# Performance work log

Measured on AMD Instinct MI355X. Metric: run time of the kernel, lower is better.

## Reference

```python
import jax, jax.numpy as jnp
import numpy as np

B, C, E = 2, 1024, 1024
H = 16            # n_heads as declared (used as per-group feature dim due to module's reshape)
HD = E // H       # 64 — the axis actually batched over in attention


def setup_inputs() -> dict:
    key = jax.random.key(0)
    ks = jax.random.split(key, 5)
    scale = 0.02
    return {
        "x": jax.random.normal(ks[0], (B, C, E), dtype=jnp.float32),
        "W_q": jax.random.normal(ks[1], (E, E), dtype=jnp.float32) * scale,
        "W_k": jax.random.normal(ks[2], (E, E), dtype=jnp.float32) * scale,
        "W_v": jax.random.normal(ks[3], (E, E), dtype=jnp.float32) * scale,
        "W_o": jax.random.normal(ks[4], (E, E), dtype=jnp.float32) * scale,
    }


def reference(x, W_q, W_k, W_v, W_o):
    # nn.Linear: y = x @ W.T  (bias=False)
    def proj_split(W):
        y = jnp.einsum('bce,de->bcd', x, W)              # [B,C,E]
        # view(B, C, HD, H).transpose(1,2) -> [B, HD, C, H]  (faithful to source layout)
        return y.reshape(B, C, HD, H).transpose(0, 2, 1, 3)

    Q = proj_split(W_q)
    K = proj_split(W_k)
    V = proj_split(W_v)

    scale = 1.0 / jnp.sqrt(jnp.asarray(H, dtype=x.dtype))  # sqrt of last dim (= n_heads here)
    scores = jnp.einsum('bdqh,bdkh->bdqk', Q, K) * scale    # [B, HD, C, C]
    weights = jax.nn.softmax(scores, axis=-1)
    out = jnp.einsum('bdqk,bdkh->bdqh', weights, V)         # [B, HD, C, H]
    out = out.transpose(0, 2, 1, 3).reshape(B, C, E)        # [B, C, E]
    out = jnp.einsum('bce,de->bcd', out, W_o)
    return out  # dropout p=0.0 / eval mode: identity
```

## Files before the change

kernel.cpp:

```cpp
#include <hip/hip_runtime.h>
#include <stdint.h>
#include <math.h>


typedef __bf16   bf16x8 __attribute__((ext_vector_type(8)));
typedef float    f32x4  __attribute__((ext_vector_type(4)));

__device__ __forceinline__ unsigned short f2bf(float f) {
    unsigned int u = __float_as_uint(f);
    u += 0x7FFFu + ((u >> 16) & 1u);
    return (unsigned short)(u >> 16);
}

__device__ __forceinline__ unsigned int pkbf(float lo, float hi) {
    const unsigned int ulo = __float_as_uint(lo) + 0x8000u;
    const unsigned int uhi = __float_as_uint(hi) + 0x8000u;
    return __builtin_amdgcn_perm(uhi, ulo, 0x07060302u);
}

__device__ __forceinline__ void gl16(const unsigned short* g, unsigned short* l) {
    __builtin_amdgcn_global_load_lds(
        (const __attribute__((address_space(1))) unsigned int*)g,
        (__attribute__((address_space(3))) unsigned int*)l, 16, 0, 0);
}

__global__ __launch_bounds__(256) void cast_to_bf16(
    const float* __restrict__ x,
    const float* __restrict__ w0, const float* __restrict__ w1,
    const float* __restrict__ w2, const float* __restrict__ w3,
    unsigned short* __restrict__ xb,
    unsigned short* __restrict__ b0, unsigned short* __restrict__ b1,
    unsigned short* __restrict__ b2, unsigned short* __restrict__ b3)
{
    const int z = blockIdx.y;
    const float* src;
    unsigned short* dst;
    size_t off = 0;
    float sc = 1.f;
    if (z < 2)       { src = x;  dst = xb; off = (size_t)z << 20; }
    else if (z == 2) { src = w0; dst = b0; sc = 0.36067376022224085f; }
    else if (z == 3) { src = w1; dst = b1; }
    else if (z == 4) { src = w2; dst = b2; }
    else             { src = w3; dst = b3; }
    const size_t i = off + ((size_t)blockIdx.x * 256 + threadIdx.x) * 4;
    const float4 v = *(const float4*)(src + i);
    *(ushort4*)(dst + i) = make_ushort4(f2bf(v.x * sc), f2bf(v.y * sc),
                                        f2bf(v.z * sc), f2bf(v.w * sc));
}

__global__ __launch_bounds__(256) void gemm128_bt_mfma(
    const unsigned short* __restrict__ A,
    const unsigned short* __restrict__ B0, const unsigned short* __restrict__ B1,
    const unsigned short* __restrict__ B2,
    unsigned short* __restrict__ C0, unsigned short* __restrict__ C1,
    unsigned short* __restrict__ C2,
    int M, int N, int K)
{
    const unsigned short* Bm = (blockIdx.z == 0) ? B0 : (blockIdx.z == 1) ? B1 : B2;
    unsigned short* Cm       = (blockIdx.z == 0) ? C0 : (blockIdx.z == 1) ? C1 : C2;

    __shared__ __align__(16) unsigned short As[2][128 * 32];
    __shared__ __align__(16) unsigned short Bs[2][128 * 32];

    const int t    = threadIdx.x;
    const int lane = t & 63;
    const int w    = t >> 6;
    const int m0   = blockIdx.y * 128;
    const int n0   = blockIdx.x * 128;
    const int wm   = (w & 1) * 64;
    const int wn   = (w >> 1) * 64;

    const int r0 = t >> 2;
    const int c0 = (t & 3) * 8;
    const unsigned short* Apa = A  + (size_t)(m0 + r0) * K + c0;
    const unsigned short* Apb = Apa + (size_t)64 * K;
    const unsigned short* Bpa = Bm + (size_t)(n0 + r0) * K + c0;
    const unsigned short* Bpb = Bpa + (size_t)64 * K;
    unsigned short* lA0 = &As[0][w * 512];
    unsigned short* lA1 = &As[0][2048 + w * 512];
    unsigned short* lB0 = &Bs[0][w * 512];
    unsigned short* lB1 = &Bs[0][2048 + w * 512];
    const int bufStr = 128 * 32;

    f32x4 acc[4][4];
#pragma unroll
    for (int i = 0; i < 4; ++i)
#pragma unroll
        for (int j = 0; j < 4; ++j) acc[i][j] = (f32x4){0.f, 0.f, 0.f, 0.f};

    const int fm = lane & 15;
    const int kg = lane >> 4;

    gl16(Apa, lA0);
    gl16(Apb, lA1);
    gl16(Bpa, lB0);
    gl16(Bpb, lB1);

    int cur = 0;
    for (int k0 = 0; k0 < K; k0 += 32) {
        __syncthreads();

        if (k0 + 32 < K) {
            const int nb = (cur ^ 1);
            gl16(Apa + k0 + 32, lA0 + nb * bufStr);
            gl16(Apb + k0 + 32, lA1 + nb * bufStr);
            gl16(Bpa + k0 + 32, lB0 + nb * bufStr);
            gl16(Bpb + k0 + 32, lB1 + nb * bufStr);
        }

        const unsigned short* Ab = &As[cur][0];
        const unsigned short* Bb = &Bs[cur][0];
        bf16x8 af[4], bfr[4];
#pragma unroll
        for (int im = 0; im < 4; ++im)
            af[im] = *(const bf16x8*)&Ab[(wm + im * 16 + fm) * 32 + kg * 8];
#pragma unroll
        for (int in = 0; in < 4; ++in)
            bfr[in] = *(const bf16x8*)&Bb[(wn + in * 16 + fm) * 32 + kg * 8];
#pragma unroll
        for (int im = 0; im < 4; ++im)
#pragma unroll
            for (int in = 0; in < 4; ++in)
                acc[im][in] = __builtin_amdgcn_mfma_f32_16x16x32_bf16(
                    af[im], bfr[in], acc[im][in], 0, 0, 0);

        cur ^= 1;
    }

#pragma unroll
    for (int im = 0; im < 4; ++im) {
#pragma unroll
        for (int in = 0; in < 4; ++in) {
            const int row = m0 + wm + im * 16 + kg * 4;
            const int col = n0 + wn + in * 16 + fm;
#pragma unroll
            for (int r = 0; r < 4; ++r)
                Cm[(size_t)(row + r) * N + col] = f2bf(acc[im][in][r]);
        }
    }
}

__global__ __launch_bounds__(256) void gemm_bt_mfma(
    const unsigned short* __restrict__ A,
    const unsigned short* __restrict__ B0, const unsigned short* __restrict__ B1,
    const unsigned short* __restrict__ B2,
    void* __restrict__ C0, void* __restrict__ C1, void* __restrict__ C2,
    int M, int N, int K, int bf16out)
{
    const unsigned short* Bm = (blockIdx.z == 0) ? B0 : (blockIdx.z == 1) ? B1 : B2;
    void* Cm                 = (blockIdx.z == 0) ? C0 : (blockIdx.z == 1) ? C1 : C2;

    __shared__ __align__(16) unsigned short As[2][64 * 32];
    __shared__ __align__(16) unsigned short Bs[2][128 * 32];

    const int t    = threadIdx.x;
    const int lane = t & 63;
    const int w    = t >> 6;
    const int m0   = blockIdx.y * 64;
    const int n0   = blockIdx.x * 128;
    const int wm   = (w & 1) * 32;
    const int wn   = (w >> 1) * 64;

    const int r0 = t >> 2;
    const int c0 = (t & 3) * 8;
    const unsigned short* Apa = A  + (size_t)(m0 + r0) * K + c0;
    const unsigned short* Bpa = Bm + (size_t)(n0 + r0) * K + c0;
    const unsigned short* Bpb = Bm + (size_t)(n0 + r0 + 64) * K + c0;
    unsigned short* ldsA  = &As[0][w * 512];
    unsigned short* ldsB0 = &Bs[0][w * 512];
    unsigned short* ldsB1 = &Bs[0][2048 + w * 512];
    const int bufStrA = 64 * 32;
    const int bufStrB = 128 * 32;

    f32x4 acc[2][4];
#pragma unroll
    for (int i = 0; i < 2; ++i)
#pragma unroll
        for (int j = 0; j < 4; ++j) acc[i][j] = (f32x4){0.f, 0.f, 0.f, 0.f};

    const int fm = lane & 15;
    const int kg = lane >> 4;

    gl16(Apa, ldsA);
    gl16(Bpa, ldsB0);
    gl16(Bpb, ldsB1);

    int cur = 0;
    for (int k0 = 0; k0 < K; k0 += 32) {
        __syncthreads();

        if (k0 + 32 < K) {
            const int nb = (cur ^ 1);
            gl16(Apa + k0 + 32, ldsA  + nb * bufStrA);
            gl16(Bpa + k0 + 32, ldsB0 + nb * bufStrB);
            gl16(Bpb + k0 + 32, ldsB1 + nb * bufStrB);
        }

        const unsigned short* Ab = &As[cur][0];
        const unsigned short* Bb = &Bs[cur][0];
        bf16x8 af[2], bfr[4];
#pragma unroll
        for (int im = 0; im < 2; ++im)
            af[im] = *(const bf16x8*)&Ab[(wm + im * 16 + fm) * 32 + kg * 8];
#pragma unroll
        for (int in = 0; in < 4; ++in)
            bfr[in] = *(const bf16x8*)&Bb[(wn + in * 16 + fm) * 32 + kg * 8];
#pragma unroll
        for (int im = 0; im < 2; ++im)
#pragma unroll
            for (int in = 0; in < 4; ++in)
                acc[im][in] = __builtin_amdgcn_mfma_f32_16x16x32_bf16(
                    af[im], bfr[in], acc[im][in], 0, 0, 0);

        cur ^= 1;
    }

#pragma unroll
    for (int im = 0; im < 2; ++im) {
#pragma unroll
        for (int in = 0; in < 4; ++in) {
            const int row = m0 + wm + im * 16 + kg * 4;
            const int col = n0 + wn + in * 16 + fm;
            if (bf16out) {
                unsigned short* cp = (unsigned short*)Cm;
#pragma unroll
                for (int r = 0; r < 4; ++r)
                    cp[(size_t)(row + r) * N + col] = f2bf(acc[im][in][r]);
            } else {
                float* cp = (float*)Cm;
#pragma unroll
                for (int r = 0; r < 4; ++r)
                    cp[(size_t)(row + r) * N + col] = acc[im][in][r];
            }
        }
    }
}

#define KSTR2 40
#define VSTR2 72
#define PSTR  80

__global__ __launch_bounds__(256) void attn_mfma(
    const unsigned short* __restrict__ Qb, const unsigned short* __restrict__ Kb,
    const unsigned short* __restrict__ Vb, unsigned short* __restrict__ Ob)
{
    __shared__ __align__(16) unsigned short Ks[64 * KSTR2];
    __shared__ __align__(16) unsigned short VsT[16 * VSTR2];
    __shared__ __align__(16) unsigned short Ps[128 * PSTR];
    __shared__ __align__(16) float Lsh[128];

    const int t    = threadIdx.x;
    const int lane = t & 63;
    const int wq   = t >> 6;
    const int fm   = lane & 15;
    const int kg   = lane >> 4;
    const int bh   = blockIdx.y;
    const size_t base = ((size_t)(bh >> 6) * 1024) * 1024 + (size_t)(bh & 63) * 16;
    const int q0 = blockIdx.x * 128;

    if (t < 128) {
        const int row = t >> 1, seg = t & 1;
        *(uint4*)&Ks[row * KSTR2 + 16 + seg * 8] = make_uint4(0, 0, 0, 0);
    }

    union { uint4 u; bf16x8 h; } zz; zz.u = make_uint4(0, 0, 0, 0);
    bf16x8 aq[2];
#pragma unroll
    for (int m = 0; m < 2; ++m) {
        if (kg < 2)
            aq[m] = *(const bf16x8*)(Qb + base +
                     (size_t)(q0 + wq * 32 + m * 16 + fm) * 1024 + kg * 8);
        else
            aq[m] = zz.h;
    }

    f32x4 oacc[2];
    float lp[2];
#pragma unroll
    for (int m = 0; m < 2; ++m) {
        oacc[m] = (f32x4){0.f, 0.f, 0.f, 0.f};
        lp[m] = 0.f;
    }

    for (int kt = 0; kt < 1024; kt += 64) {
        __syncthreads();
        if (t < 128) {
            const int row = t >> 1, seg = t & 1;
            *(uint4*)&Ks[row * KSTR2 + seg * 8] =
                *(const uint4*)(Kb + base + (size_t)(kt + row) * 1024 + seg * 8);
        } else {
            const int idx = t - 128;
            const int key = idx >> 1, half = idx & 1;
            uint4 v = *(const uint4*)(Vb + base + (size_t)(kt + key) * 1024 + half * 8);
            const unsigned short* pv = (const unsigned short*)&v;
#pragma unroll
            for (int d = 0; d < 8; ++d)
                VsT[(half * 8 + d) * VSTR2 + key] = pv[d];
        }
        __syncthreads();

        bf16x8 bk[4];
#pragma unroll
        for (int kn = 0; kn < 4; ++kn)
            bk[kn] = *(const bf16x8*)&Ks[(kn * 16 + fm) * KSTR2 + kg * 8];

#pragma unroll
        for (int kn = 0; kn < 4; ++kn) {
            f32x4 sm[2];
#pragma unroll
            for (int m = 0; m < 2; ++m)
                sm[m] = __builtin_amdgcn_mfma_f32_16x16x32_bf16(
                    bk[kn], aq[m], (f32x4){0.f, 0.f, 0.f, 0.f}, 0, 0, 0);
#pragma unroll
            for (int m = 0; m < 2; ++m) {
                const float p0 = __builtin_amdgcn_exp2f(sm[m][0]);
                const float p1 = __builtin_amdgcn_exp2f(sm[m][1]);
                const float p2 = __builtin_amdgcn_exp2f(sm[m][2]);
                const float p3 = __builtin_amdgcn_exp2f(sm[m][3]);
                lp[m] += (p0 + p1) + (p2 + p3);
                *(uint2*)&Ps[(wq * 32 + m * 16 + fm) * PSTR + kn * 16 + kg * 4] =
                    make_uint2(pkbf(p0, p1), pkbf(p2, p3));
            }
        }

        bf16x8 bv0 = *(const bf16x8*)&VsT[fm * VSTR2 + kg * 8];
        bf16x8 bv1 = *(const bf16x8*)&VsT[fm * VSTR2 + 32 + kg * 8];
#pragma unroll
        for (int m = 0; m < 2; ++m) {
            const int prow = wq * 32 + m * 16 + fm;
            bf16x8 ap0 = *(const bf16x8*)&Ps[prow * PSTR + kg * 8];
            bf16x8 ap1 = *(const bf16x8*)&Ps[prow * PSTR + 32 + kg * 8];
            oacc[m] = __builtin_amdgcn_mfma_f32_16x16x32_bf16(ap0, bv0, oacc[m], 0, 0, 0);
            oacc[m] = __builtin_amdgcn_mfma_f32_16x16x32_bf16(ap1, bv1, oacc[m], 0, 0, 0);
        }
    }

#pragma unroll
    for (int m = 0; m < 2; ++m) {
        float v = lp[m];
        v += __shfl_xor(v, 16, 64);
        v += __shfl_xor(v, 32, 64);
        if (kg == 0) Lsh[wq * 32 + m * 16 + fm] = v;
    }

#pragma unroll
    for (int m = 0; m < 2; ++m) {
        const float4 lr = *(const float4*)&Lsh[wq * 32 + m * 16 + kg * 4];
        const int qrow = q0 + wq * 32 + m * 16 + kg * 4;
        Ob[base + (size_t)(qrow + 0) * 1024 + fm] = f2bf(oacc[m][0] / lr.x);
        Ob[base + (size_t)(qrow + 1) * 1024 + fm] = f2bf(oacc[m][1] / lr.y);
        Ob[base + (size_t)(qrow + 2) * 1024 + fm] = f2bf(oacc[m][2] / lr.z);
        Ob[base + (size_t)(qrow + 3) * 1024 + fm] = f2bf(oacc[m][3] / lr.w);
    }
}

extern "C" void kernel_launch(void* const* d_in, const int* in_sizes, int n_in,
                              void* d_out, int out_size, void* d_ws, size_t ws_size,
                              hipStream_t stream) {
    const float* x  = (const float*)d_in[0];
    const float* Wq = (const float*)d_in[1];
    const float* Wk = (const float*)d_in[2];
    const float* Wv = (const float*)d_in[3];
    const float* Wo = (const float*)d_in[4];
    float* out = (float*)d_out;

    const int M = 2048, N = 1024, Kd = 1024;
    const size_t MEG = 1048576;
    unsigned short* ws = (unsigned short*)d_ws;
    unsigned short* xb  = ws;
    unsigned short* Wqb = ws + 2 * MEG;
    unsigned short* Wkb = ws + 3 * MEG;
    unsigned short* Wvb = ws + 4 * MEG;
    unsigned short* Wob = ws + 5 * MEG;
    unsigned short* Qb  = ws + 6 * MEG;
    unsigned short* Kb  = ws + 8 * MEG;
    unsigned short* Vb  = ws + 10 * MEG;
    unsigned short* Ob  = ws + 12 * MEG;

    dim3 gc(1024, 6, 1);
    cast_to_bf16<<<gc, 256, 0, stream>>>(x, Wq, Wk, Wv, Wo, xb, Wqb, Wkb, Wvb, Wob);

    dim3 g1(N / 128, M / 128, 3);
    gemm128_bt_mfma<<<g1, 256, 0, stream>>>(xb, Wqb, Wkb, Wvb, Qb, Kb, Vb, M, N, Kd);

    dim3 g2(8, 128, 1);
    attn_mfma<<<g2, 256, 0, stream>>>(Qb, Kb, Vb, Ob);

    dim3 g3(N / 128, M / 64, 1);
    gemm_bt_mfma<<<g3, 256, 0, stream>>>(Ob, Wob, Wob, Wob, out, out, out, M, N, Kd, 0);
}
```

Measured before the change: 156.7 us.

## Split attention key tiles across waves and reduce partial outputs through LDS

The attention kernel now splits each 128-key tile across the four waves, so every wave handles all 128 query rows for its own 32 keys. Previously each wave owned 32 query rows and walked all 64 keys of a smaller tile. Partial outputs and row sums are combined at the end through a shared-memory reduction. Doubling the key tile halves the number of loop iterations and barriers, all threads now take part in loading K and V, and P is packed to bf16 with a hardware convert instruction instead of bit tricks. In exchange the kernel uses more registers and shared memory (occupancy hint of 3 blocks per SIMD) and adds an end-of-kernel cross-wave reduction.

```diff
diff --git a/kernel.cpp b/kernel.cpp
--- a/kernel.cpp
+++ b/kernel.cpp
@@ -12,10 +12,10 @@
     return (unsigned short)(u >> 16);
 }
 
-__device__ __forceinline__ unsigned int pkbf(float lo, float hi) {
-    const unsigned int ulo = __float_as_uint(lo) + 0x8000u;
-    const unsigned int uhi = __float_as_uint(hi) + 0x8000u;
-    return __builtin_amdgcn_perm(uhi, ulo, 0x07060302u);
+__device__ __forceinline__ unsigned int cvtpk(float lo, float hi) {
+    unsigned int r;
+    asm("v_cvt_pk_bf16_f32 %0, %1, %2" : "=v"(r) : "v"(lo), "v"(hi));
+    return r;
 }
 
 __device__ __forceinline__ void gl16(const unsigned short* g, unsigned short* l) {
@@ -236,121 +236,127 @@
     }
 }
 
-#define KSTR2 40
-#define VSTR2 72
-#define PSTR  80
-
-__global__ __launch_bounds__(256) void attn_mfma(
+#define KSTR  40
+#define VSTRD 136
+#define PSTRD 136
+
+__global__ __launch_bounds__(256, 3) void attn_mfma(
     const unsigned short* __restrict__ Qb, const unsigned short* __restrict__ Kb,
     const unsigned short* __restrict__ Vb, unsigned short* __restrict__ Ob)
 {
-    __shared__ __align__(16) unsigned short Ks[64 * KSTR2];
-    __shared__ __align__(16) unsigned short VsT[16 * VSTR2];
-    __shared__ __align__(16) unsigned short Ps[128 * PSTR];
-    __shared__ __align__(16) float Lsh[128];
+    __shared__ __align__(16) unsigned char smem[49408];
+    unsigned short* Ks  = (unsigned short*)smem;
+    unsigned short* VsT = (unsigned short*)(smem + 10240);
+    unsigned short* Ps  = (unsigned short*)(smem + 14592);
+    float*          Red = (float*)smem;
 
     const int t    = threadIdx.x;
     const int lane = t & 63;
-    const int wq   = t >> 6;
+    const int wv   = t >> 6;
     const int fm   = lane & 15;
     const int kg   = lane >> 4;
     const int bh   = blockIdx.y;
-    const size_t base = ((size_t)(bh >> 6) * 1024) * 1024 + (size_t)(bh & 63) * 16;
+    const size_t base = ((size_t)(bh >> 6) << 20) + (size_t)(bh & 63) * 16;
     const int q0 = blockIdx.x * 128;
-
-    if (t < 128) {
+    const int wk = wv * 32;
+
+    {
         const int row = t >> 1, seg = t & 1;
-        *(uint4*)&Ks[row * KSTR2 + 16 + seg * 8] = make_uint4(0, 0, 0, 0);
+        *(uint4*)&Ks[row * KSTR + 16 + seg * 8] = make_uint4(0, 0, 0, 0);
     }
 
     union { uint4 u; bf16x8 h; } zz; zz.u = make_uint4(0, 0, 0, 0);
-    bf16x8 aq[2];
-#pragma unroll
-    for (int m = 0; m < 2; ++m) {
+    bf16x8 aq[8];
+#pragma unroll
+    for (int m = 0; m < 8; ++m) {
         if (kg < 2)
             aq[m] = *(const bf16x8*)(Qb + base +
-                     (size_t)(q0 + wq * 32 + m * 16 + fm) * 1024 + kg * 8);
+                     (size_t)(q0 + m * 16 + fm) * 1024 + kg * 8);
         else
             aq[m] = zz.h;
     }
 
-    f32x4 oacc[2];
-    float lp[2];
-#pragma unroll
-    for (int m = 0; m < 2; ++m) {
+    f32x4 oacc[8];
+    float lp[8];
+#pragma unroll
+    for (int m = 0; m < 8; ++m) {
         oacc[m] = (f32x4){0.f, 0.f, 0.f, 0.f};
         lp[m] = 0.f;
     }
 
-    for (int kt = 0; kt < 1024; kt += 64) {
+    for (int kt = 0; kt < 1024; kt += 128) {
         __syncthreads();
-        if (t < 128) {
+        {
             const int row = t >> 1, seg = t & 1;
-            *(uint4*)&Ks[row * KSTR2 + seg * 8] =
+            *(uint4*)&Ks[row * KSTR + seg * 8] =
                 *(const uint4*)(Kb + base + (size_t)(kt + row) * 1024 + seg * 8);
-        } else {
-            const int idx = t - 128;
-            const int key = idx >> 1, half = idx & 1;
-            uint4 v = *(const uint4*)(Vb + base + (size_t)(kt + key) * 1024 + half * 8);
+            uint4 v = *(const uint4*)(Vb + base + (size_t)(kt + row) * 1024 + seg * 8);
             const unsigned short* pv = (const unsigned short*)&v;
 #pragma unroll
             for (int d = 0; d < 8; ++d)
-                VsT[(half * 8 + d) * VSTR2 + key] = pv[d];
+                VsT[(seg * 8 + d) * VSTRD + row] = pv[d];
         }
         __syncthreads();
 
-        bf16x8 bk[4];
-#pragma unroll
-        for (int kn = 0; kn < 4; ++kn)
-            bk[kn] = *(const bf16x8*)&Ks[(kn * 16 + fm) * KSTR2 + kg * 8];
-
-#pragma unroll
-        for (int kn = 0; kn < 4; ++kn) {
-            f32x4 sm[2];
-#pragma unroll
-            for (int m = 0; m < 2; ++m)
-                sm[m] = __builtin_amdgcn_mfma_f32_16x16x32_bf16(
-                    bk[kn], aq[m], (f32x4){0.f, 0.f, 0.f, 0.f}, 0, 0, 0);
-#pragma unroll
-            for (int m = 0; m < 2; ++m) {
-                const float p0 = __builtin_amdgcn_exp2f(sm[m][0]);
-                const float p1 = __builtin_amdgcn_exp2f(sm[m][1]);
-                const float p2 = __builtin_amdgcn_exp2f(sm[m][2]);
-                const float p3 = __builtin_amdgcn_exp2f(sm[m][3]);
-                lp[m] += (p0 + p1) + (p2 + p3);
-                *(uint2*)&Ps[(wq * 32 + m * 16 + fm) * PSTR + kn * 16 + kg * 4] =
-                    make_uint2(pkbf(p0, p1), pkbf(p2, p3));
-            }
-        }
-
-        bf16x8 bv0 = *(const bf16x8*)&VsT[fm * VSTR2 + kg * 8];
-        bf16x8 bv1 = *(const bf16x8*)&VsT[fm * VSTR2 + 32 + kg * 8];
-#pragma unroll
-        for (int m = 0; m < 2; ++m) {
-            const int prow = wq * 32 + m * 16 + fm;
-            bf16x8 ap0 = *(const bf16x8*)&Ps[prow * PSTR + kg * 8];
-            bf16x8 ap1 = *(const bf16x8*)&Ps[prow * PSTR + 32 + kg * 8];
-            oacc[m] = __builtin_amdgcn_mfma_f32_16x16x32_bf16(ap0, bv0, oacc[m], 0, 0, 0);
-            oacc[m] = __builtin_amdgcn_mfma_f32_16x16x32_bf16(ap1, bv1, oacc[m], 0, 0, 0);
-        }
-    }
-
-#pragma unroll
-    for (int m = 0; m < 2; ++m) {
-        float v = lp[m];
-        v += __shfl_xor(v, 16, 64);
-        v += __shfl_xor(v, 32, 64);
-        if (kg == 0) Lsh[wq * 32 + m * 16 + fm] = v;
-    }
-
-#pragma unroll
-    for (int m = 0; m < 2; ++m) {
-        const float4 lr = *(const float4*)&Lsh[wq * 32 + m * 16 + kg * 4];
-        const int qrow = q0 + wq * 32 + m * 16 + kg * 4;
-        Ob[base + (size_t)(qrow + 0) * 1024 + fm] = f2bf(oacc[m][0] / lr.x);
-        Ob[base + (size_t)(qrow + 1) * 1024 + fm] = f2bf(oacc[m][1] / lr.y);
-        Ob[base + (size_t)(qrow + 2) * 1024 + fm] = f2bf(oacc[m][2] / lr.z);
-        Ob[base + (size_t)(qrow + 3) * 1024 + fm] = f2bf(oacc[m][3] / lr.w);
+        const bf16x8 bk0 = *(const bf16x8*)&Ks[(wk + fm) * KSTR + kg * 8];
+        const bf16x8 bk1 = *(const bf16x8*)&Ks[(wk + 16 + fm) * KSTR + kg * 8];
+
+#pragma unroll
+        for (int m = 0; m < 8; ++m) {
+            f32x4 s0 = __builtin_amdgcn_mfma_f32_16x16x32_bf16(
+                bk0, aq[m], (f32x4){0.f, 0.f, 0.f, 0.f}, 0, 0, 0);
+            f32x4 s1 = __builtin_amdgcn_mfma_f32_16x16x32_bf16(
+                bk1, aq[m], (f32x4){0.f, 0.f, 0.f, 0.f}, 0, 0, 0);
+            const float p0 = __builtin_amdgcn_exp2f(s0[0]);
+            const float p1 = __builtin_amdgcn_exp2f(s0[1]);
+            const float p2 = __builtin_amdgcn_exp2f(s0[2]);
+            const float p3 = __builtin_amdgcn_exp2f(s0[3]);
+            const float p4 = __builtin_amdgcn_exp2f(s1[0]);
+            const float p5 = __builtin_amdgcn_exp2f(s1[1]);
+            const float p6 = __builtin_amdgcn_exp2f(s1[2]);
+            const float p7 = __builtin_amdgcn_exp2f(s1[3]);
+            lp[m] += ((p0 + p1) + (p2 + p3)) + ((p4 + p5) + (p6 + p7));
+            unsigned short* prow = &Ps[(m * 16 + fm) * PSTRD + wk];
+            *(uint2*)&prow[kg * 4]      = make_uint2(cvtpk(p0, p1), cvtpk(p2, p3));
+            *(uint2*)&prow[16 + kg * 4] = make_uint2(cvtpk(p4, p5), cvtpk(p6, p7));
+        }
+
+        const bf16x8 bv = *(const bf16x8*)&VsT[fm * VSTRD + wk + kg * 8];
+#pragma unroll
+        for (int m = 0; m < 8; ++m) {
+            const bf16x8 ap = *(const bf16x8*)&Ps[(m * 16 + fm) * PSTRD + wk + kg * 8];
+            oacc[m] = __builtin_amdgcn_mfma_f32_16x16x32_bf16(ap, bv, oacc[m], 0, 0, 0);
+        }
+    }
+
+#pragma unroll
+    for (int m = 0; m < 8; ++m) {
+        lp[m] += __shfl_xor(lp[m], 16, 64);
+        lp[m] += __shfl_xor(lp[m], 32, 64);
+    }
+
+    __syncthreads();
+#pragma unroll
+    for (int m = 0; m < 8; ++m) {
+#pragma unroll
+        for (int r = 0; r < 4; ++r)
+            Red[((wv * 128) + m * 16 + kg * 4 + r) * 17 + fm] = oacc[m][r];
+        if (kg == 0)
+            Red[((wv * 128) + m * 16 + fm) * 17 + 16] = lp[m];
+    }
+    __syncthreads();
+
+#pragma unroll
+    for (int mp = 0; mp < 2; ++mp) {
+#pragma unroll
+        for (int r = 0; r < 4; ++r) {
+            const int q = wv * 32 + mp * 16 + kg * 4 + r;
+            const float o = Red[q * 17 + fm]         + Red[(128 + q) * 17 + fm] +
+                            Red[(256 + q) * 17 + fm] + Red[(384 + q) * 17 + fm];
+            const float l = Red[q * 17 + 16]         + Red[(128 + q) * 17 + 16] +
+                            Red[(256 + q) * 17 + 16] + Red[(384 + q) * 17 + 16];
+            Ob[base + (size_t)(q0 + q) * 1024 + fm] = f2bf(o / l);
+        }
     }
 }
 
```

New measurement: 153.3 us. 2.1% less time.
